# Kernel optimization log

Hardware: AMD Instinct MI355X
Metric: run time of the kernel (lower is better)

The kernel has to match this reference:

```python
import jax, jax.numpy as jnp
import numpy as np

N = 200_000          # nodes (chain graph)
E = N - 1            # edges = diff structure
F = 5                # node features: [pos, vel_hist(3), cur_vel]
L = 16               # latent_size
G = 2                # globals: [time, static_param]
D = 3 * L + G        # ODE state dim = node_lat + sent_agg + recv_agg + globals
NSTEPS = 4           # fixed RK4 steps standing in for adaptive Tsit5 over t in [0,1]
DT = 0.01            # integrator dt of the physics post-processor


def setup_inputs() -> dict:
    key = jax.random.key(0)
    ks = iter(jax.random.split(key, 32))
    s = 0.1  # small init so the ODE stays well-behaved
    p = lambda shape: jax.random.normal(next(ks), shape, jnp.float32) * s
    inp = {}
    inp["nodes"] = jax.random.normal(next(ks), (N, F), jnp.float32)
    inp["edges"] = jax.random.normal(next(ks), (E, 1), jnp.float32)
    inp["g"] = jnp.zeros((G,), jnp.float32)
    inp["enc_n_w1"] = p((F, L)); inp["enc_n_b1"] = jnp.zeros((L,), jnp.float32)
    inp["enc_n_w2"] = p((L, L)); inp["enc_n_b2"] = jnp.zeros((L,), jnp.float32)
    inp["enc_e_w1"] = p((1, L)); inp["enc_e_b1"] = jnp.zeros((L,), jnp.float32)
    inp["enc_e_w2"] = p((L, L)); inp["enc_e_b2"] = jnp.zeros((L,), jnp.float32)
    inp["ode_w1"] = p((D + 1, D)); inp["ode_b1"] = jnp.zeros((D,), jnp.float32)
    inp["ode_w2"] = p((D, D)); inp["ode_b2"] = jnp.zeros((D,), jnp.float32)
    inp["node_out_w"] = p((D, L)); inp["node_out_b"] = jnp.zeros((L,), jnp.float32)
    inp["dec_n_w1"] = p((L, L)); inp["dec_n_b1"] = jnp.zeros((L,), jnp.float32)
    inp["dec_n_w2"] = p((L, L)); inp["dec_n_b2"] = jnp.zeros((L,), jnp.float32)
    inp["dec_n_w3"] = p((L, 1)); inp["dec_n_b3"] = jnp.zeros((1,), jnp.float32)
    inp["senders"] = jnp.arange(E, dtype=jnp.int32)
    inp["receivers"] = jnp.arange(1, N, dtype=jnp.int32)
    return inp


def reference(nodes, edges, g,
              enc_n_w1, enc_n_b1, enc_n_w2, enc_n_b2,
              enc_e_w1, enc_e_b1, enc_e_w2, enc_e_b2,
              ode_w1, ode_b1, ode_w2, ode_b2,
              node_out_w, node_out_b,
              dec_n_w1, dec_n_b1, dec_n_w2, dec_n_b2, dec_n_w3, dec_n_b3,
              senders, receivers):
    swish = jax.nn.swish
    n = nodes.shape[0]
    cur_pos = nodes[:, 0]
    cur_vel = nodes[:, -1]

    # --- encoder: MLP [L, L] on nodes and edges (swish, no final act) ---
    nlat = swish(nodes @ enc_n_w1 + enc_n_b1) @ enc_n_w2 + enc_n_b2   # [N, L]
    elat = swish(edges @ enc_e_w1 + enc_e_b1) @ enc_e_w2 + enc_e_b2   # [E, L]

    # --- processor (1 MP step): gather/scatter + Neural-ODE node update ---
    sent = jax.ops.segment_sum(elat, senders, num_segments=n)        # [N, L]
    recv = jax.ops.segment_sum(elat, receivers, num_segments=n)      # [N, L]
    gb = jnp.broadcast_to(g, (n, g.shape[0]))                        # [N, G]
    y0 = jnp.concatenate([nlat, sent, recv, gb], axis=1)             # [N, D]

    def f(t, y):  # derivative net: relu MLP on concat(y, t)
        inp = jnp.concatenate([y, jnp.full((y.shape[0], 1), t, y.dtype)], axis=1)
        return jax.nn.relu(inp @ ode_w1 + ode_b1) @ ode_w2 + ode_b2

    h = jnp.float32(1.0 / NSTEPS)

    def step(carry, _):
        y, t = carry
        k1 = f(t, y)
        k2 = f(t + 0.5 * h, y + 0.5 * h * k1)
        k3 = f(t + 0.5 * h, y + 0.5 * h * k2)
        k4 = f(t + h, y + h * k3)
        y = y + (h / 6.0) * (k1 + 2.0 * k2 + 2.0 * k3 + k4)
        return (y, t + h), None

    (yT, _), _ = jax.lax.scan(step, (y0, jnp.float32(0.0)), None, length=NSTEPS)
    nlat2 = yT @ node_out_w + node_out_b                             # [N, L]

    # --- global update: increment time ---
    g_new = jnp.concatenate([g[:1] + 1.0, g[1:]])

    # --- decoder node MLP [L, L, 1] ---
    dh = swish(nlat2 @ dec_n_w1 + dec_n_b1)
    dh = swish(dh @ dec_n_w2 + dec_n_b2)
    pred_acc = (dh @ dec_n_w3 + dec_n_b3).reshape(-1)                # [N]

    # --- semi-implicit Euler post-processor ---
    next_vel = cur_vel + pred_acc * DT
    next_pos = cur_pos + next_vel * DT
    next_nodes = jnp.column_stack([next_pos, nodes[:, 2:], next_vel, pred_acc])
    next_edges = jnp.diff(next_pos).reshape(-1, 1)
    return next_nodes, next_edges, g_new
```

## Files before the change

kernel.cpp:

```cpp
#include <hip/hip_runtime.h>

#define NN 200000
#define EE (NN - 1)
#define NSTEPS 4
#define DTC 0.01f
#define WPB 4
#define NPB 128
#define GRID 1563

typedef __attribute__((ext_vector_type(8))) _Float16 f16x8;
typedef __attribute__((ext_vector_type(2))) _Float16 f16x2;
typedef __attribute__((ext_vector_type(4))) float f32x4;

struct H4 { f16x2 a, b, c, d; };

__device__ __forceinline__ f16x2 c2h(float lo, float hi) {
    return __builtin_bit_cast(f16x2, __builtin_amdgcn_cvt_pkrtz(lo, hi));
}
__device__ __forceinline__ unsigned pk2h(float lo, float hi) {
    return __builtin_bit_cast(unsigned, __builtin_amdgcn_cvt_pkrtz(lo, hi));
}
__device__ __forceinline__ f16x8 h8(f16x2 a, f16x2 b, f16x2 c, f16x2 d) {
    H4 t{a, b, c, d};
    return __builtin_bit_cast(f16x8, t);
}
__device__ __forceinline__ f16x2 relu2(f16x2 v) {
    f16x2 r;
    asm("v_pk_max_f16 %0, %1, 0" : "=v"(r) : "v"(v));
    return r;
}
__device__ __forceinline__ float swishf(float x) { return x / (1.0f + __expf(-x)); }

__device__ __forceinline__ int permk(int k) {
    return (k & 0x23) | ((k & 4) << 2) | ((k & 0x18) >> 1);
}

__device__ __forceinline__ f16x8 setw(f16x8 v, bool cond, unsigned nw) {
    uint4 u = __builtin_bit_cast(uint4, v);
    u.w = cond ? nw : u.w;
    return __builtin_bit_cast(f16x8, u);
}

__global__ void gnode_weights(const float* __restrict__ ode_w1, const float* __restrict__ ode_b1,
                              const float* __restrict__ ode_w2, const float* __restrict__ ode_b2,
                              const float* __restrict__ enc_n_w2, const float* __restrict__ enc_e_w2,
                              const float* __restrict__ dec_n_w1, const float* __restrict__ dec_n_w2,
                              const float* __restrict__ node_out_w,
                              unsigned short* __restrict__ wg)
{
    const int b = blockIdx.x;
    const int tid = threadIdx.x;
    if (b < 8) {
        const int i = tid + b * 256;
        const int od = i >> 5;
        const int k2 = (i & 31) * 2;
        const int s0 = permk(k2);
        const int s1 = s0 + 1;
        float a0 = 0.f, a1 = 0.f, b0 = 0.f, b1 = 0.f;
        if (od < 50) {
            a0 = (s0 <= 50) ? ode_w1[s0 * 50 + od] : 0.f;
            a1 = (s1 <= 50) ? ode_w1[s1 * 50 + od]
                            : ((s1 == 51) ? ode_b1[od] : 0.f);
            b0 = (s0 < 50) ? ode_w2[s0 * 50 + od]
                           : ((s0 == 50) ? ode_b2[od] : 0.f);
            b1 = (s1 < 50) ? ode_w2[s1 * 50 + od] : 0.f;
        }
        const int ct = od >> 4;
        const int mm = od & 15;
        const int kt = k2 >> 5;
        const int qq = (k2 >> 3) & 3;
        const int jj = k2 & 7;
        const int didx = ct * 1024 + kt * 512 + (mm * 4 + qq) * 8 + jj;
        *(unsigned*)(wg + didx) = pk2h(a0, a1);
        *(unsigned*)(wg + 4096 + didx) = pk2h(b0, b1);
    } else if (b < 10) {
        const int i = tid + (b - 8) * 256;
        const int mm = i >> 5;
        const int kp = (i & 31) * 2;
        const int s0 = permk(kp);
        const float v0 = (s0     < 50) ? node_out_w[s0 * 16 + mm] : 0.f;
        const float v1 = (s0 + 1 < 50) ? node_out_w[(s0 + 1) * 16 + mm] : 0.f;
        *(unsigned*)(wg + 10240 + mm * 64 + kp) = pk2h(v0, v1);
    } else {
        const int mm = tid >> 4;
        const int kp = (tid & 15) * 2;
        const bool rl = (kp < 16);
        const float eN0 = rl ? enc_n_w2[kp * 16 + mm] : 0.f;
        const float eN1 = rl ? enc_n_w2[(kp + 1) * 16 + mm] : 0.f;
        const float eE0 = rl ? enc_e_w2[kp * 16 + mm] : 0.f;
        const float eE1 = rl ? enc_e_w2[(kp + 1) * 16 + mm] : 0.f;
        const float d10 = rl ? dec_n_w1[kp * 16 + mm] : 0.f;
        const float d11 = rl ? dec_n_w1[(kp + 1) * 16 + mm] : 0.f;
        const float d20 = rl ? dec_n_w2[kp * 16 + mm] : 0.f;
        const float d21 = rl ? dec_n_w2[(kp + 1) * 16 + mm] : 0.f;
        *(unsigned*)(wg + 8192 + mm * 32 + kp) = pk2h(eN0, eN1);
        *(unsigned*)(wg + 8704 + mm * 32 + kp) = pk2h(eE0, eE1);
        *(unsigned*)(wg + 9216 + mm * 32 + kp) = pk2h(d10, d11);
        *(unsigned*)(wg + 9728 + mm * 32 + kp) = pk2h(d20, d21);
    }
}

__global__ __launch_bounds__(256, 3)
void gnode_main(const float* __restrict__ nodes,
                const float* __restrict__ edges,
                const float* __restrict__ g,
                const float* __restrict__ enc_n_w1, const float* __restrict__ enc_n_b1,
                const float* __restrict__ enc_n_b2,
                const float* __restrict__ enc_e_w1, const float* __restrict__ enc_e_b1,
                const float* __restrict__ enc_e_b2,
                const float* __restrict__ node_out_b,
                const float* __restrict__ dec_n_b1, const float* __restrict__ dec_n_b2,
                const float* __restrict__ dec_n_w3, const float* __restrict__ dec_n_b3,
                const unsigned short* __restrict__ wg,
                float* __restrict__ out, float* __restrict__ npos)
{
    __shared__ __attribute__((aligned(16))) unsigned short dscr[WPB][640];
    __shared__ __attribute__((aligned(16))) unsigned short sw[8192];

    const int tid  = threadIdx.x;
    const int lane = tid & 63;
    const int wave = __builtin_amdgcn_readfirstlane(tid >> 6);
    const int m = lane & 15;
    const int q = lane >> 4;
    const bool q0 = (q == 0);
    unsigned short* const dscrw = &dscr[wave][0];

#pragma unroll
    for (int i = 0; i < 4; ++i)
        ((uint4*)sw)[tid + 256 * i] = ((const uint4*)wg)[tid + 256 * i];

    int nd[2], nc[2];
    nd[0] = blockIdx.x * NPB + wave * 32 + m;
    nd[1] = nd[0] + 16;
    nc[0] = (nd[0] < NN) ? nd[0] : (NN - 1);
    nc[1] = (nd[1] < NN) ? nd[1] : (NN - 1);

    *(uint2*)(dscrw + m * 40 + 16 + q * 4) = make_uint2(0u, 0u);

    const f32x4 zero4 = {0.f, 0.f, 0.f, 0.f};
    const f16x2 h2z = {(_Float16)0.f, (_Float16)0.f};
    const f16x8 z8 = h8(h2z, h2z, h2z, h2z);

    f16x8 Y[2][2], ACC[2][2], A[2][2];

    {
        const f16x8 wNf = *(const f16x8*)(const void*)(wg + 8192 + m * 32 + q * 8);
        const f16x8 wEf = *(const f16x8*)(const void*)(wg + 8704 + m * 32 + q * 8);
        f32x4 bN, bE;
#pragma unroll
        for (int r = 0; r < 4; ++r) { bN[r] = enc_n_b2[q * 4 + r]; bE[r] = enc_e_b2[q * 4 + r]; }
        const float g0v = g[0], g1v = g[1];

#pragma unroll
        for (int tt = 0; tt < 2; ++tt) {
            const int node = nc[tt];
            f32x4 e0, e1, e2;
            {
                float nf[5];
#pragma unroll
                for (int c = 0; c < 5; ++c) nf[c] = nodes[node * 5 + c];
                f16x8 bfr = z8;
                if (q < 2) {
                    float hv[8];
#pragma unroll
                    for (int j = 0; j < 8; ++j) {
                        const int d = q * 8 + j;
                        float s = enc_n_b1[d];
#pragma unroll
                        for (int c = 0; c < 5; ++c) s = fmaf(nf[c], enc_n_w1[c * 16 + d], s);
                        hv[j] = swishf(s);
                    }
                    bfr = h8(c2h(hv[0], hv[1]), c2h(hv[2], hv[3]),
                             c2h(hv[4], hv[5]), c2h(hv[6], hv[7]));
                }
                e0 = __builtin_amdgcn_mfma_f32_16x16x32_f16(wNf, bfr, bN, 0, 0, 0);
            }
            {
                const float ev = (node < EE) ? edges[node] : 0.0f;
                f16x8 bfr = z8;
                if (q < 2) {
                    float hv[8];
#pragma unroll
                    for (int j = 0; j < 8; ++j) {
                        const int d = q * 8 + j;
                        hv[j] = swishf(fmaf(ev, enc_e_w1[d], enc_e_b1[d]));
                    }
                    bfr = h8(c2h(hv[0], hv[1]), c2h(hv[2], hv[3]),
                             c2h(hv[4], hv[5]), c2h(hv[6], hv[7]));
                }
                e1 = __builtin_amdgcn_mfma_f32_16x16x32_f16(wEf, bfr, bE, 0, 0, 0);
                if (node == NN - 1) e1 = zero4;
            }
            {
                const float ev = (node > 0) ? edges[node - 1] : 0.0f;
                f16x8 bfr = z8;
                if (q < 2) {
                    float hv[8];
#pragma unroll
                    for (int j = 0; j < 8; ++j) {
                        const int d = q * 8 + j;
                        hv[j] = swishf(fmaf(ev, enc_e_w1[d], enc_e_b1[d]));
                    }
                    bfr = h8(c2h(hv[0], hv[1]), c2h(hv[2], hv[3]),
                             c2h(hv[4], hv[5]), c2h(hv[6], hv[7]));
                }
                e2 = __builtin_amdgcn_mfma_f32_16x16x32_f16(wEf, bfr, bE, 0, 0, 0);
                if (node == 0) e2 = zero4;
            }
            Y[tt][0] = h8(c2h(e0[0], e0[1]), c2h(e0[2], e0[3]),
                          c2h(e1[0], e1[1]), c2h(e1[2], e1[3]));
            Y[tt][1] = h8(c2h(e2[0], e2[1]), c2h(e2[2], e2[3]),
                          q0 ? c2h(g0v, g1v) : h2z, h2z);
            A[tt][0] = Y[tt][0];
            A[tt][1] = setw(Y[tt][1], q0, pk2h(0.f, 1.f));
        }
    }

    __syncthreads();

    const unsigned short* const swl = sw + (m * 4 + q) * 8;

    const float hh = 1.0f / NSTEPS;
    float t0 = 0.0f;
    const unsigned one2 = 0x3C003C00u;

#pragma clang loop unroll(disable)
    for (int stage = 0; stage < 4 * NSTEPS; ++stage) {
        const int s = stage & 3;

        f32x4 hc[2][4];
#pragma unroll
        for (int ct = 0; ct < 4; ++ct) {
            const f16x8 wa = *(const f16x8*)(const void*)(swl + ct * 1024);
            const f16x8 wb = *(const f16x8*)(const void*)(swl + ct * 1024 + 512);
            f32x4 c0 = __builtin_amdgcn_mfma_f32_16x16x32_f16(wa, A[0][0], zero4, 0, 0, 0);
            f32x4 c1 = __builtin_amdgcn_mfma_f32_16x16x32_f16(wa, A[1][0], zero4, 0, 0, 0);
            hc[0][ct] = __builtin_amdgcn_mfma_f32_16x16x32_f16(wb, A[0][1], c0, 0, 0, 0);
            hc[1][ct] = __builtin_amdgcn_mfma_f32_16x16x32_f16(wb, A[1][1], c1, 0, 0, 0);
        }
        f16x8 H[2][2];
#pragma unroll
        for (int tt = 0; tt < 2; ++tt) {
            H[tt][0] = h8(relu2(c2h(hc[tt][0][0], hc[tt][0][1])),
                          relu2(c2h(hc[tt][0][2], hc[tt][0][3])),
                          relu2(c2h(hc[tt][1][0], hc[tt][1][1])),
                          relu2(c2h(hc[tt][1][2], hc[tt][1][3])));
            f16x8 h1 = h8(relu2(c2h(hc[tt][2][0], hc[tt][2][1])),
                          relu2(c2h(hc[tt][2][2], hc[tt][2][3])),
                          relu2(c2h(hc[tt][3][0], hc[tt][3][1])),
                          relu2(c2h(hc[tt][3][2], hc[tt][3][3])));
            H[tt][1] = setw(h1, q0, one2);
        }
        f32x4 kc[2][4];
#pragma unroll
        for (int ct = 0; ct < 4; ++ct) {
            const f16x8 wa = *(const f16x8*)(const void*)(swl + 4096 + ct * 1024);
            const f16x8 wb = *(const f16x8*)(const void*)(swl + 4096 + ct * 1024 + 512);
            f32x4 c0 = __builtin_amdgcn_mfma_f32_16x16x32_f16(wa, H[0][0], zero4, 0, 0, 0);
            f32x4 c1 = __builtin_amdgcn_mfma_f32_16x16x32_f16(wa, H[1][0], zero4, 0, 0, 0);
            kc[0][ct] = __builtin_amdgcn_mfma_f32_16x16x32_f16(wb, H[0][1], c0, 0, 0, 0);
            kc[1][ct] = __builtin_amdgcn_mfma_f32_16x16x32_f16(wb, H[1][1], c1, 0, 0, 0);
        }

        const float ca = (s == 0 || s == 3) ? hh / 6.0f : hh / 3.0f;
        const float cb = (s == 2) ? hh : 0.5f * hh;
        const f16x2 cah = c2h(ca, ca);
        const f16x2 cbh = c2h(cb, cb);
        const f16x8 ca8 = h8(cah, cah, cah, cah);
        const f16x8 cb8 = h8(cbh, cbh, cbh, cbh);
        float tn;
        if (s < 3) tn = t0 + cb;
        else { t0 += hh; tn = t0; }
        const unsigned tw = pk2h(tn, 1.0f);

#pragma unroll
        for (int tt = 0; tt < 2; ++tt) {
            f16x8 KC0 = h8(c2h(kc[tt][0][0], kc[tt][0][1]), c2h(kc[tt][0][2], kc[tt][0][3]),
                           c2h(kc[tt][1][0], kc[tt][1][1]), c2h(kc[tt][1][2], kc[tt][1][3]));
            f16x8 KC1 = h8(c2h(kc[tt][2][0], kc[tt][2][1]), c2h(kc[tt][2][2], kc[tt][2][3]),
                           c2h(kc[tt][3][0], kc[tt][3][1]), c2h(kc[tt][3][2], kc[tt][3][3]));
            if (s == 0) {
                ACC[tt][0] = ca8 * KC0 + Y[tt][0];
                ACC[tt][1] = ca8 * KC1 + Y[tt][1];
            } else {
                ACC[tt][0] = ca8 * KC0 + ACC[tt][0];
                ACC[tt][1] = ca8 * KC1 + ACC[tt][1];
            }
            f16x8 av0, av1;
            if (s < 3) {
                av0 = cb8 * KC0 + Y[tt][0];
                av1 = cb8 * KC1 + Y[tt][1];
            } else {
                Y[tt][0] = ACC[tt][0];
                Y[tt][1] = ACC[tt][1];
                av0 = ACC[tt][0];
                av1 = ACC[tt][1];
            }
            A[tt][0] = av0;
            A[tt][1] = setw(av1, q0, tw);
        }
    }

    const f16x8 dw1 = *(const f16x8*)(const void*)(wg + 9216 + m * 32 + q * 8);
    const f16x8 dw2 = *(const f16x8*)(const void*)(wg + 9728 + m * 32 + q * 8);
    const f16x8 ow0 = *(const f16x8*)(const void*)(wg + 10240 + m * 64 + q * 8);
    const f16x8 ow1 = *(const f16x8*)(const void*)(wg + 10240 + m * 64 + 32 + q * 8);
    f32x4 bO, bD1, bD2;
    float w3v[4];
#pragma unroll
    for (int r = 0; r < 4; ++r) {
        bO[r]  = node_out_b[q * 4 + r];
        bD1[r] = dec_n_b1[q * 4 + r];
        bD2[r] = dec_n_b2[q * 4 + r];
        w3v[r] = dec_n_w3[q * 4 + r];
    }

#pragma unroll
    for (int tt = 0; tt < 2; ++tt) {
        f32x4 nl2 = __builtin_amdgcn_mfma_f32_16x16x32_f16(ow0, Y[tt][0], bO, 0, 0, 0);
        nl2       = __builtin_amdgcn_mfma_f32_16x16x32_f16(ow1, Y[tt][1], nl2, 0, 0, 0);

        *(uint2*)(dscrw + m * 40 + q * 4) =
            make_uint2(pk2h(nl2[0], nl2[1]), pk2h(nl2[2], nl2[3]));
        f16x8 nB = *(const f16x8*)(const void*)(dscrw + m * 40 + q * 8);
        f32x4 dh = __builtin_amdgcn_mfma_f32_16x16x32_f16(dw1, nB, bD1, 0, 0, 0);
#pragma unroll
        for (int r = 0; r < 4; ++r) dh[r] = swishf(dh[r]);

        *(uint2*)(dscrw + m * 40 + q * 4) =
            make_uint2(pk2h(dh[0], dh[1]), pk2h(dh[2], dh[3]));
        f16x8 dB = *(const f16x8*)(const void*)(dscrw + m * 40 + q * 8);
        f32x4 dh2 = __builtin_amdgcn_mfma_f32_16x16x32_f16(dw2, dB, bD2, 0, 0, 0);
#pragma unroll
        for (int r = 0; r < 4; ++r) dh2[r] = swishf(dh2[r]);

        float p = dh2[0] * w3v[0];
        p = fmaf(dh2[1], w3v[1], p);
        p = fmaf(dh2[2], w3v[2], p);
        p = fmaf(dh2[3], w3v[3], p);
        p += __shfl_xor(p, 16);
        p += __shfl_xor(p, 32);
        p += dec_n_b3[0];

        const int node = nd[tt];
        if (q0 && node < NN) {
            const float cur_pos = nodes[node * 5 + 0];
            const float c2 = nodes[node * 5 + 2];
            const float c3 = nodes[node * 5 + 3];
            const float cur_vel = nodes[node * 5 + 4];
            const float next_vel = fmaf(p, DTC, cur_vel);
            const float next_pos = fmaf(next_vel, DTC, cur_pos);
            out[node * 6 + 0] = next_pos;
            out[node * 6 + 1] = c2;
            out[node * 6 + 2] = c3;
            out[node * 6 + 3] = cur_vel;
            out[node * 6 + 4] = next_vel;
            out[node * 6 + 5] = p;
            npos[node] = next_pos;
        }
    }
}

__global__ void gnode_edges(const float* __restrict__ npos,
                            float* __restrict__ out,
                            const float* __restrict__ g)
{
    const int e = blockIdx.x * blockDim.x + threadIdx.x;
    if (e < EE) {
        out[NN * 6 + e] = npos[e + 1] - npos[e];
    }
    if (e == 0) {
        out[NN * 6 + EE]     = g[0] + 1.0f;
        out[NN * 6 + EE + 1] = g[1];
    }
}

extern "C" void kernel_launch(void* const* d_in, const int* in_sizes, int n_in,
                              void* d_out, int out_size, void* d_ws, size_t ws_size,
                              hipStream_t stream) {
    const float* nodes      = (const float*)d_in[0];
    const float* edges      = (const float*)d_in[1];
    const float* g          = (const float*)d_in[2];
    const float* enc_n_w1   = (const float*)d_in[3];
    const float* enc_n_b1   = (const float*)d_in[4];
    const float* enc_n_w2   = (const float*)d_in[5];
    const float* enc_n_b2   = (const float*)d_in[6];
    const float* enc_e_w1   = (const float*)d_in[7];
    const float* enc_e_b1   = (const float*)d_in[8];
    const float* enc_e_w2   = (const float*)d_in[9];
    const float* enc_e_b2   = (const float*)d_in[10];
    const float* ode_w1     = (const float*)d_in[11];
    const float* ode_b1     = (const float*)d_in[12];
    const float* ode_w2     = (const float*)d_in[13];
    const float* ode_b2     = (const float*)d_in[14];
    const float* node_out_w = (const float*)d_in[15];
    const float* node_out_b = (const float*)d_in[16];
    const float* dec_n_w1   = (const float*)d_in[17];
    const float* dec_n_b1   = (const float*)d_in[18];
    const float* dec_n_w2   = (const float*)d_in[19];
    const float* dec_n_b2   = (const float*)d_in[20];
    const float* dec_n_w3   = (const float*)d_in[21];
    const float* dec_n_b3   = (const float*)d_in[22];
    float* out  = (float*)d_out;
    float* npos = (float*)d_ws;
    unsigned short* wg = (unsigned short*)((char*)d_ws + (size_t)NN * 4);

    gnode_weights<<<11, 256, 0, stream>>>(
        ode_w1, ode_b1, ode_w2, ode_b2,
        enc_n_w2, enc_e_w2, dec_n_w1, dec_n_w2, node_out_w, wg);

    gnode_main<<<GRID, 256, 0, stream>>>(
        nodes, edges, g,
        enc_n_w1, enc_n_b1, enc_n_b2,
        enc_e_w1, enc_e_b1, enc_e_b2,
        node_out_b, dec_n_b1, dec_n_b2, dec_n_w3, dec_n_b3,
        wg, out, npos);

    gnode_edges<<<(EE + 255) / 256, 256, 0, stream>>>(npos, out, g);
}
```

Before: 172.0 us.

## Fuse weight prep and edge diff into single main kernel with overlapping tiles

```diff
diff --git a/kernel.cpp b/kernel.cpp
--- a/kernel.cpp
+++ b/kernel.cpp
@@ -5,8 +5,8 @@
 #define NSTEPS 4
 #define DTC 0.01f
 #define WPB 4
-#define NPB 128
-#define GRID 1563
+#define NSTR 127
+#define GRID 1575
 
 typedef __attribute__((ext_vector_type(8))) _Float16 f16x8;
 typedef __attribute__((ext_vector_type(2))) _Float16 f16x2;
@@ -41,17 +41,43 @@
     return __builtin_bit_cast(f16x8, u);
 }
 
-__global__ void gnode_weights(const float* __restrict__ ode_w1, const float* __restrict__ ode_b1,
-                              const float* __restrict__ ode_w2, const float* __restrict__ ode_b2,
-                              const float* __restrict__ enc_n_w2, const float* __restrict__ enc_e_w2,
-                              const float* __restrict__ dec_n_w1, const float* __restrict__ dec_n_w2,
-                              const float* __restrict__ node_out_w,
-                              unsigned short* __restrict__ wg)
+__global__ __launch_bounds__(256, 3)
+void gnode_main(const float* __restrict__ nodes,
+                const float* __restrict__ edges,
+                const float* __restrict__ g,
+                const float* __restrict__ enc_n_w1, const float* __restrict__ enc_n_b1,
+                const float* __restrict__ enc_n_w2, const float* __restrict__ enc_n_b2,
+                const float* __restrict__ enc_e_w1, const float* __restrict__ enc_e_b1,
+                const float* __restrict__ enc_e_w2, const float* __restrict__ enc_e_b2,
+                const float* __restrict__ ode_w1, const float* __restrict__ ode_b1,
+                const float* __restrict__ ode_w2, const float* __restrict__ ode_b2,
+                const float* __restrict__ node_out_w, const float* __restrict__ node_out_b,
+                const float* __restrict__ dec_n_w1, const float* __restrict__ dec_n_b1,
+                const float* __restrict__ dec_n_w2, const float* __restrict__ dec_n_b2,
+                const float* __restrict__ dec_n_w3, const float* __restrict__ dec_n_b3,
+                float* __restrict__ out)
 {
-    const int b = blockIdx.x;
-    const int tid = threadIdx.x;
-    if (b < 8) {
-        const int i = tid + b * 256;
+    __shared__ __attribute__((aligned(16))) unsigned short sw[8192];
+    __shared__ __attribute__((aligned(16))) unsigned short senc[512];
+    __shared__ __attribute__((aligned(16))) unsigned short sene[512];
+    __shared__ __attribute__((aligned(16))) unsigned short sd1[512];
+    __shared__ __attribute__((aligned(16))) unsigned short sd2[512];
+    __shared__ __attribute__((aligned(16))) unsigned short sout[1024];
+    __shared__ __attribute__((aligned(16))) unsigned short dscr[WPB][640];
+    __shared__ float pos_s[128];
+
+    const int tid  = threadIdx.x;
+    const int lane = tid & 63;
+    const int wave = __builtin_amdgcn_readfirstlane(tid >> 6);
+    const int m = lane & 15;
+    const int q = lane >> 4;
+    const bool q0 = (q == 0);
+    unsigned short* const dscrw = &dscr[wave][0];
+    const int base = blockIdx.x * NSTR;
+
+#pragma unroll
+    for (int it = 0; it < 8; ++it) {
+        const int i = tid + it * 256;
         const int od = i >> 5;
         const int k2 = (i & 31) * 2;
         const int s0 = permk(k2);
@@ -71,17 +97,20 @@
         const int qq = (k2 >> 3) & 3;
         const int jj = k2 & 7;
         const int didx = ct * 1024 + kt * 512 + (mm * 4 + qq) * 8 + jj;
-        *(unsigned*)(wg + didx) = pk2h(a0, a1);
-        *(unsigned*)(wg + 4096 + didx) = pk2h(b0, b1);
-    } else if (b < 10) {
-        const int i = tid + (b - 8) * 256;
+        *(unsigned*)(sw + didx) = pk2h(a0, a1);
+        *(unsigned*)(sw + 4096 + didx) = pk2h(b0, b1);
+    }
+#pragma unroll
+    for (int it = 0; it < 2; ++it) {
+        const int i = tid + it * 256;
         const int mm = i >> 5;
         const int kp = (i & 31) * 2;
         const int s0 = permk(kp);
         const float v0 = (s0     < 50) ? node_out_w[s0 * 16 + mm] : 0.f;
         const float v1 = (s0 + 1 < 50) ? node_out_w[(s0 + 1) * 16 + mm] : 0.f;
-        *(unsigned*)(wg + 10240 + mm * 64 + kp) = pk2h(v0, v1);
-    } else {
+        *(unsigned*)(sout + mm * 64 + kp) = pk2h(v0, v1);
+    }
+    {
         const int mm = tid >> 4;
         const int kp = (tid & 15) * 2;
         const bool rl = (kp < 16);
@@ -93,50 +122,24 @@
         const float d11 = rl ? dec_n_w1[(kp + 1) * 16 + mm] : 0.f;
         const float d20 = rl ? dec_n_w2[kp * 16 + mm] : 0.f;
         const float d21 = rl ? dec_n_w2[(kp + 1) * 16 + mm] : 0.f;
-        *(unsigned*)(wg + 8192 + mm * 32 + kp) = pk2h(eN0, eN1);
-        *(unsigned*)(wg + 8704 + mm * 32 + kp) = pk2h(eE0, eE1);
-        *(unsigned*)(wg + 9216 + mm * 32 + kp) = pk2h(d10, d11);
-        *(unsigned*)(wg + 9728 + mm * 32 + kp) = pk2h(d20, d21);
-    }
-}
-
-__global__ __launch_bounds__(256, 3)
-void gnode_main(const float* __restrict__ nodes,
-                const float* __restrict__ edges,
-                const float* __restrict__ g,
-                const float* __restrict__ enc_n_w1, const float* __restrict__ enc_n_b1,
-                const float* __restrict__ enc_n_b2,
-                const float* __restrict__ enc_e_w1, const float* __restrict__ enc_e_b1,
-                const float* __restrict__ enc_e_b2,
-                const float* __restrict__ node_out_b,
-                const float* __restrict__ dec_n_b1, const float* __restrict__ dec_n_b2,
-                const float* __restrict__ dec_n_w3, const float* __restrict__ dec_n_b3,
-                const unsigned short* __restrict__ wg,
-                float* __restrict__ out, float* __restrict__ npos)
-{
-    __shared__ __attribute__((aligned(16))) unsigned short dscr[WPB][640];
-    __shared__ __attribute__((aligned(16))) unsigned short sw[8192];
-
-    const int tid  = threadIdx.x;
-    const int lane = tid & 63;
-    const int wave = __builtin_amdgcn_readfirstlane(tid >> 6);
-    const int m = lane & 15;
-    const int q = lane >> 4;
-    const bool q0 = (q == 0);
-    unsigned short* const dscrw = &dscr[wave][0];
-
-#pragma unroll
-    for (int i = 0; i < 4; ++i)
-        ((uint4*)sw)[tid + 256 * i] = ((const uint4*)wg)[tid + 256 * i];
-
-    int nd[2], nc[2];
-    nd[0] = blockIdx.x * NPB + wave * 32 + m;
+        *(unsigned*)(senc + mm * 32 + kp) = pk2h(eN0, eN1);
+        *(unsigned*)(sene + mm * 32 + kp) = pk2h(eE0, eE1);
+        *(unsigned*)(sd1 + mm * 32 + kp) = pk2h(d10, d11);
+        *(unsigned*)(sd2 + mm * 32 + kp) = pk2h(d20, d21);
+    }
+
+    int nd[2], nc[2], loc[2];
+    loc[0] = wave * 32 + m;
+    loc[1] = loc[0] + 16;
+    nd[0] = base + loc[0];
     nd[1] = nd[0] + 16;
     nc[0] = (nd[0] < NN) ? nd[0] : (NN - 1);
     nc[1] = (nd[1] < NN) ? nd[1] : (NN - 1);
 
     *(uint2*)(dscrw + m * 40 + 16 + q * 4) = make_uint2(0u, 0u);
 
+    __syncthreads();
+
     const f32x4 zero4 = {0.f, 0.f, 0.f, 0.f};
     const f16x2 h2z = {(_Float16)0.f, (_Float16)0.f};
     const f16x8 z8 = h8(h2z, h2z, h2z, h2z);
@@ -144,12 +147,11 @@
     f16x8 Y[2][2], ACC[2][2], A[2][2];
 
     {
-        const f16x8 wNf = *(const f16x8*)(const void*)(wg + 8192 + m * 32 + q * 8);
-        const f16x8 wEf = *(const f16x8*)(const void*)(wg + 8704 + m * 32 + q * 8);
+        const f16x8 wNf = *(const f16x8*)(const void*)(senc + m * 32 + q * 8);
+        const f16x8 wEf = *(const f16x8*)(const void*)(sene + m * 32 + q * 8);
         f32x4 bN, bE;
 #pragma unroll
         for (int r = 0; r < 4; ++r) { bN[r] = enc_n_b2[q * 4 + r]; bE[r] = enc_e_b2[q * 4 + r]; }
-        const float g0v = g[0], g1v = g[1];
 
 #pragma unroll
         for (int tt = 0; tt < 2; ++tt) {
@@ -207,6 +209,7 @@
                 e2 = __builtin_amdgcn_mfma_f32_16x16x32_f16(wEf, bfr, bE, 0, 0, 0);
                 if (node == 0) e2 = zero4;
             }
+            const float g0v = g[0], g1v = g[1];
             Y[tt][0] = h8(c2h(e0[0], e0[1]), c2h(e0[2], e0[3]),
                           c2h(e1[0], e1[1]), c2h(e1[2], e1[3]));
             Y[tt][1] = h8(c2h(e2[0], e2[1]), c2h(e2[2], e2[3]),
@@ -215,8 +218,6 @@
             A[tt][1] = setw(Y[tt][1], q0, pk2h(0.f, 1.f));
         }
     }
-
-    __syncthreads();
 
     const unsigned short* const swl = sw + (m * 4 + q) * 8;
 
@@ -301,10 +302,10 @@
         }
     }
 
-    const f16x8 dw1 = *(const f16x8*)(const void*)(wg + 9216 + m * 32 + q * 8);
-    const f16x8 dw2 = *(const f16x8*)(const void*)(wg + 9728 + m * 32 + q * 8);
-    const f16x8 ow0 = *(const f16x8*)(const void*)(wg + 10240 + m * 64 + q * 8);
-    const f16x8 ow1 = *(const f16x8*)(const void*)(wg + 10240 + m * 64 + 32 + q * 8);
+    const f16x8 dw1 = *(const f16x8*)(const void*)(sd1 + m * 32 + q * 8);
+    const f16x8 dw2 = *(const f16x8*)(const void*)(sd2 + m * 32 + q * 8);
+    const f16x8 ow0 = *(const f16x8*)(const void*)(sout + m * 64 + q * 8);
+    const f16x8 ow1 = *(const f16x8*)(const void*)(sout + m * 64 + 32 + q * 8);
     f32x4 bO, bD1, bD2;
     float w3v[4];
 #pragma unroll
@@ -343,33 +344,32 @@
         p += dec_n_b3[0];
 
         const int node = nd[tt];
-        if (q0 && node < NN) {
-            const float cur_pos = nodes[node * 5 + 0];
-            const float c2 = nodes[node * 5 + 2];
-            const float c3 = nodes[node * 5 + 3];
-            const float cur_vel = nodes[node * 5 + 4];
+        if (q0) {
+            const float cur_pos = nodes[nc[tt] * 5 + 0];
+            const float cur_vel = nodes[nc[tt] * 5 + 4];
             const float next_vel = fmaf(p, DTC, cur_vel);
             const float next_pos = fmaf(next_vel, DTC, cur_pos);
-            out[node * 6 + 0] = next_pos;
-            out[node * 6 + 1] = c2;
-            out[node * 6 + 2] = c3;
-            out[node * 6 + 3] = cur_vel;
-            out[node * 6 + 4] = next_vel;
-            out[node * 6 + 5] = p;
-            npos[node] = next_pos;
-        }
-    }
-}
-
-__global__ void gnode_edges(const float* __restrict__ npos,
-                            float* __restrict__ out,
-                            const float* __restrict__ g)
-{
-    const int e = blockIdx.x * blockDim.x + threadIdx.x;
-    if (e < EE) {
-        out[NN * 6 + e] = npos[e + 1] - npos[e];
-    }
-    if (e == 0) {
+            pos_s[loc[tt]] = next_pos;
+            if (node < NN && loc[tt] < NSTR) {
+                const float c2 = nodes[node * 5 + 2];
+                const float c3 = nodes[node * 5 + 3];
+                out[node * 6 + 0] = next_pos;
+                out[node * 6 + 1] = c2;
+                out[node * 6 + 2] = c3;
+                out[node * 6 + 3] = cur_vel;
+                out[node * 6 + 4] = next_vel;
+                out[node * 6 + 5] = p;
+            }
+        }
+    }
+
+    __syncthreads();
+
+    if (tid < NSTR) {
+        const int e = base + tid;
+        if (e < EE) out[NN * 6 + e] = pos_s[tid + 1] - pos_s[tid];
+    }
+    if (blockIdx.x == 0 && tid == 0) {
         out[NN * 6 + EE]     = g[0] + 1.0f;
         out[NN * 6 + EE + 1] = g[1];
     }
@@ -402,19 +402,13 @@
     const float* dec_n_w3   = (const float*)d_in[21];
     const float* dec_n_b3   = (const float*)d_in[22];
     float* out  = (float*)d_out;
-    float* npos = (float*)d_ws;
-    unsigned short* wg = (unsigned short*)((char*)d_ws + (size_t)NN * 4);
-
-    gnode_weights<<<11, 256, 0, stream>>>(
-        ode_w1, ode_b1, ode_w2, ode_b2,
-        enc_n_w2, enc_e_w2, dec_n_w1, dec_n_w2, node_out_w, wg);
 
     gnode_main<<<GRID, 256, 0, stream>>>(
         nodes, edges, g,
-        enc_n_w1, enc_n_b1, enc_n_b2,
-        enc_e_w1, enc_e_b1, enc_e_b2,
-        node_out_b, dec_n_b1, dec_n_b2, dec_n_w3, dec_n_b3,
-        wg, out, npos);
-
-    gnode_edges<<<(EE + 255) / 256, 256, 0, stream>>>(npos, out, g);
-}
+        enc_n_w1, enc_n_b1, enc_n_w2, enc_n_b2,
+        enc_e_w1, enc_e_b1, enc_e_w2, enc_e_b2,
+        ode_w1, ode_b1, ode_w2, ode_b2,
+        node_out_w, node_out_b,
+        dec_n_w1, dec_n_b1, dec_n_w2, dec_n_b2, dec_n_w3, dec_n_b3,
+        out);
+}
```

Measured after the change: 171.8 us. Within noise of the previous version (-0.1%).

## Fuse edge-diff kernel into main kernel using overlapping node tiles

Applied to the files above, without the earlier changes.

```diff
diff --git a/kernel.cpp b/kernel.cpp
--- a/kernel.cpp
+++ b/kernel.cpp
@@ -5,8 +5,8 @@
 #define NSTEPS 4
 #define DTC 0.01f
 #define WPB 4
-#define NPB 128
-#define GRID 1563
+#define NSTR 127
+#define GRID 1575
 
 typedef __attribute__((ext_vector_type(8))) _Float16 f16x8;
 typedef __attribute__((ext_vector_type(2))) _Float16 f16x2;
@@ -70,7 +70,7 @@
         const int kt = k2 >> 5;
         const int qq = (k2 >> 3) & 3;
         const int jj = k2 & 7;
-        const int didx = ct * 1024 + kt * 512 + (mm * 4 + qq) * 8 + jj;
+        const int didx = ct * 1024 + kt * 512 + (qq * 16 + mm) * 8 + jj;
         *(unsigned*)(wg + didx) = pk2h(a0, a1);
         *(unsigned*)(wg + 4096 + didx) = pk2h(b0, b1);
     } else if (b < 10) {
@@ -112,10 +112,11 @@
                 const float* __restrict__ dec_n_b1, const float* __restrict__ dec_n_b2,
                 const float* __restrict__ dec_n_w3, const float* __restrict__ dec_n_b3,
                 const unsigned short* __restrict__ wg,
-                float* __restrict__ out, float* __restrict__ npos)
+                float* __restrict__ out)
 {
     __shared__ __attribute__((aligned(16))) unsigned short dscr[WPB][640];
     __shared__ __attribute__((aligned(16))) unsigned short sw[8192];
+    __shared__ float pos_s[128];
 
     const int tid  = threadIdx.x;
     const int lane = tid & 63;
@@ -124,13 +125,16 @@
     const int q = lane >> 4;
     const bool q0 = (q == 0);
     unsigned short* const dscrw = &dscr[wave][0];
+    const int base = blockIdx.x * NSTR;
 
 #pragma unroll
     for (int i = 0; i < 4; ++i)
         ((uint4*)sw)[tid + 256 * i] = ((const uint4*)wg)[tid + 256 * i];
 
-    int nd[2], nc[2];
-    nd[0] = blockIdx.x * NPB + wave * 32 + m;
+    int nd[2], nc[2], loc[2];
+    loc[0] = wave * 32 + m;
+    loc[1] = loc[0] + 16;
+    nd[0] = base + loc[0];
     nd[1] = nd[0] + 16;
     nc[0] = (nd[0] < NN) ? nd[0] : (NN - 1);
     nc[1] = (nd[1] < NN) ? nd[1] : (NN - 1);
@@ -218,7 +222,7 @@
 
     __syncthreads();
 
-    const unsigned short* const swl = sw + (m * 4 + q) * 8;
+    const unsigned short* const swl = sw + (q * 16 + m) * 8;
 
     const float hh = 1.0f / NSTEPS;
     float t0 = 0.0f;
@@ -343,33 +347,32 @@
         p += dec_n_b3[0];
 
         const int node = nd[tt];
-        if (q0 && node < NN) {
-            const float cur_pos = nodes[node * 5 + 0];
-            const float c2 = nodes[node * 5 + 2];
-            const float c3 = nodes[node * 5 + 3];
-            const float cur_vel = nodes[node * 5 + 4];
+        if (q0) {
+            const float cur_pos = nodes[nc[tt] * 5 + 0];
+            const float cur_vel = nodes[nc[tt] * 5 + 4];
             const float next_vel = fmaf(p, DTC, cur_vel);
             const float next_pos = fmaf(next_vel, DTC, cur_pos);
-            out[node * 6 + 0] = next_pos;
-            out[node * 6 + 1] = c2;
-            out[node * 6 + 2] = c3;
-            out[node * 6 + 3] = cur_vel;
-            out[node * 6 + 4] = next_vel;
-            out[node * 6 + 5] = p;
-            npos[node] = next_pos;
-        }
-    }
-}
-
-__global__ void gnode_edges(const float* __restrict__ npos,
-                            float* __restrict__ out,
-                            const float* __restrict__ g)
-{
-    const int e = blockIdx.x * blockDim.x + threadIdx.x;
-    if (e < EE) {
-        out[NN * 6 + e] = npos[e + 1] - npos[e];
-    }
-    if (e == 0) {
+            pos_s[loc[tt]] = next_pos;
+            if (node < NN && loc[tt] < NSTR) {
+                const float c2 = nodes[node * 5 + 2];
+                const float c3 = nodes[node * 5 + 3];
+                out[node * 6 + 0] = next_pos;
+                out[node * 6 + 1] = c2;
+                out[node * 6 + 2] = c3;
+                out[node * 6 + 3] = cur_vel;
+                out[node * 6 + 4] = next_vel;
+                out[node * 6 + 5] = p;
+            }
+        }
+    }
+
+    __syncthreads();
+
+    if (tid < NSTR) {
+        const int e = base + tid;
+        if (e < EE) out[NN * 6 + e] = pos_s[tid + 1] - pos_s[tid];
+    }
+    if (blockIdx.x == 0 && tid == 0) {
         out[NN * 6 + EE]     = g[0] + 1.0f;
         out[NN * 6 + EE + 1] = g[1];
     }
@@ -402,8 +405,7 @@
     const float* dec_n_w3   = (const float*)d_in[21];
     const float* dec_n_b3   = (const float*)d_in[22];
     float* out  = (float*)d_out;
-    float* npos = (float*)d_ws;
-    unsigned short* wg = (unsigned short*)((char*)d_ws + (size_t)NN * 4);
+    unsigned short* wg = (unsigned short*)d_ws;
 
     gnode_weights<<<11, 256, 0, stream>>>(
         ode_w1, ode_b1, ode_w2, ode_b2,
@@ -414,7 +416,5 @@
         enc_n_w1, enc_n_b1, enc_n_b2,
         enc_e_w1, enc_e_b1, enc_e_b2,
         node_out_b, dec_n_b1, dec_n_b2, dec_n_w3, dec_n_b3,
-        wg, out, npos);
-
-    gnode_edges<<<(EE + 255) / 256, 256, 0, stream>>>(npos, out, g);
-}
+        wg, out);
+}
```

Result: no change. 170.1 us (-1.1%).
